# Optimization experiments

Hardware: AMD Instinct MI355X
Metric: run time of the kernel (lower is better)

Reference implementation:

```python
import jax, jax.numpy as jnp
import numpy as np

K = 3            # kernel size
PAD = 1          # padding for kernel_size=3
EPS = 1e-5       # BatchNorm eps
B, C, H, W = 8, 64, 256, 256


def deform_conv2d(x, offset, weight):
    """torchvision-style deform_conv2d, stride=1, pad=1, 1 offset group, no bias.
    x: [B, Cin, H, W]; offset: [B, 2*K*K, H, W] interleaved (dy, dx) per tap;
    weight: [Cout, Cin, K, K]."""
    b, cin, h, w = x.shape
    k2 = K * K
    off = offset.reshape(b, k2, 2, h, w)
    dy, dx = off[:, :, 0], off[:, :, 1]                 # [B,K2,H,W]
    kh = jnp.repeat(jnp.arange(K), K).astype(x.dtype)   # tap row, torch order k=kh*K+kw
    kw = jnp.tile(jnp.arange(K), K).astype(x.dtype)     # tap col
    # sampling positions: out pixel (i,j), tap k -> (i - PAD + kh + dy, j - PAD + kw + dx)
    py = dy + (jnp.arange(h, dtype=x.dtype) - PAD)[None, None, :, None] + kh[None, :, None, None]
    px = dx + (jnp.arange(w, dtype=x.dtype) - PAD)[None, None, None, :] + kw[None, :, None, None]

    y0 = jnp.floor(py); x0 = jnp.floor(px)
    wy = py - y0; wx = px - x0                          # bilinear fractions
    iy0 = y0.astype(jnp.int32); ix0 = x0.astype(jnp.int32)
    iy1 = iy0 + 1; ix1 = ix0 + 1

    xf = x.reshape(b, cin, h * w)

    def gather(iy, ix):
        valid = ((iy >= 0) & (iy < h) & (ix >= 0) & (ix < w)).astype(x.dtype)
        idx = jnp.clip(iy, 0, h - 1) * w + jnp.clip(ix, 0, w - 1)   # [B,K2,H,W]
        v = jax.vmap(lambda xi, ii: xi[:, ii])(xf, idx.reshape(b, -1))  # [B,Cin,K2*H*W]
        return v.reshape(b, cin, k2, h, w) * valid[:, None]

    sampled = ((1 - wy) * (1 - wx))[:, None] * gather(iy0, ix0) \
            + ((1 - wy) * wx)[:, None]       * gather(iy0, ix1) \
            + (wy * (1 - wx))[:, None]       * gather(iy1, ix0) \
            + (wy * wx)[:, None]             * gather(iy1, ix1)   # [B,Cin,K2,H,W]

    wk = weight.reshape(weight.shape[0], cin, k2)
    return jnp.einsum('bckhw,ock->bohw', sampled, wk)


def setup_inputs() -> dict:
    key = jax.random.key(0)
    k1, k2, k3 = jax.random.split(key, 3)
    x = jax.random.normal(k1, (B, C, H, W), dtype=jnp.float32)
    offset = jax.random.normal(k2, (B, 2 * K * K, H, W), dtype=jnp.float32)
    weight = jax.random.normal(k3, (1, 2, K, K), dtype=jnp.float32) * 0.1  # Conv2d(2,1,3)
    gamma = jnp.ones((1,), dtype=jnp.float32)
    beta = jnp.zeros((1,), dtype=jnp.float32)
    return {"x": x, "offset": offset, "weight": weight, "gamma": gamma, "beta": beta}


def reference(x, offset, weight, gamma, beta):
    avg_out = jnp.mean(x, axis=1, keepdims=True)
    max_out = jnp.max(x, axis=1, keepdims=True)
    feat = jnp.concatenate([avg_out, max_out], axis=1)      # [B,2,H,W]
    out = deform_conv2d(feat, offset, weight)               # [B,1,H,W]
    # BatchNorm2d (training-mode batch statistics)
    mu = jnp.mean(out, axis=(0, 2, 3), keepdims=True)
    var = jnp.var(out, axis=(0, 2, 3), keepdims=True)
    out = gamma.reshape(1, -1, 1, 1) * (out - mu) * jax.lax.rsqrt(var + EPS) + beta.reshape(1, -1, 1, 1)
    return x * jax.nn.sigmoid(out)
```

## Files before the change

### kernel.cpp

```cpp
#include <hip/hip_runtime.h>
#include <math.h>

#define BB 8
#define CC 64
#define HH 256
#define WW 256
#define HWp (HH * WW)
#define BHW (BB * HWp)
#define NK 9

typedef float f32x4 __attribute__((ext_vector_type(4)));

__global__ __launch_bounds__(256) void reduce_c_kernel(
    const float* __restrict__ x, float* __restrict__ feat, float* __restrict__ accum) {
    int t = blockIdx.x * 256 + threadIdx.x;
    if (blockIdx.x == 0 && threadIdx.x < 2) accum[threadIdx.x] = 0.f;
    int b = t / (HWp / 4);
    int p = t - b * (HWp / 4);
    const f32x4* xp = reinterpret_cast<const f32x4*>(x) + (size_t)b * CC * (HWp / 4) + p;
    f32x4 s = {0.f, 0.f, 0.f, 0.f};
    f32x4 m = {-INFINITY, -INFINITY, -INFINITY, -INFINITY};
#pragma unroll 16
    for (int c = 0; c < CC; ++c) {
        f32x4 v = xp[(size_t)c * (HWp / 4)];
        s += v;
        m.x = fmaxf(m.x, v.x); m.y = fmaxf(m.y, v.y);
        m.z = fmaxf(m.z, v.z); m.w = fmaxf(m.w, v.w);
    }
    const float inv = 1.0f / CC;
    f32x4 o0 = {s.x * inv, m.x, s.y * inv, m.y};
    f32x4 o1 = {s.z * inv, m.z, s.w * inv, m.w};
    f32x4* fp = reinterpret_cast<f32x4*>(feat) + 2 * (size_t)t;
    __builtin_nontemporal_store(o0, fp);
    __builtin_nontemporal_store(o1, fp + 1);
}

__device__ __forceinline__ float2 bisample(const float2* __restrict__ f, int iy, int ix) {
    bool v = ((unsigned)iy < (unsigned)HH) && ((unsigned)ix < (unsigned)WW);
    int cy = iy < 0 ? 0 : (iy > HH - 1 ? HH - 1 : iy);
    int cx = ix < 0 ? 0 : (ix > WW - 1 ? WW - 1 : ix);
    float2 r = f[cy * WW + cx];
    return v ? r : make_float2(0.f, 0.f);
}

__global__ __launch_bounds__(256) void dconv_kernel(
    const float* __restrict__ off, const float* __restrict__ wgt,
    const float* __restrict__ feat, float* __restrict__ outmap,
    float* __restrict__ accum) {
    int t = blockIdx.x * 256 + threadIdx.x;
    int b = t >> 16;
    int p = t & (HWp - 1);
    int h = p >> 8;
    int w = p & (WW - 1);

    const float* ob = off + (size_t)b * (2 * NK) * HWp + p;
    const float2* f = reinterpret_cast<const float2*>(feat) + (size_t)b * HWp;

    float wk[2 * NK];
#pragma unroll
    for (int i = 0; i < 2 * NK; ++i) wk[i] = wgt[i];

    float acc = 0.f;
#pragma unroll
    for (int k = 0; k < NK; ++k) {
        float dy = ob[(size_t)(2 * k) * HWp];
        float dx = ob[(size_t)(2 * k + 1) * HWp];
        float py = dy + (float)(h - 1 + k / 3);
        float px = dx + (float)(w - 1 + k % 3);
        float y0 = floorf(py), x0 = floorf(px);
        float wy = py - y0, wx = px - x0;
        int iy0 = (int)y0, ix0 = (int)x0;
        float w00 = (1.f - wy) * (1.f - wx);
        float w01 = (1.f - wy) * wx;
        float w10 = wy * (1.f - wx);
        float w11 = wy * wx;
        float2 c00 = bisample(f, iy0, ix0);
        float2 c01 = bisample(f, iy0, ix0 + 1);
        float2 c10 = bisample(f, iy0 + 1, ix0);
        float2 c11 = bisample(f, iy0 + 1, ix0 + 1);
        float s0 = w00 * c00.x + w01 * c01.x + w10 * c10.x + w11 * c11.x;
        float s1 = w00 * c00.y + w01 * c01.y + w10 * c10.y + w11 * c11.y;
        acc += wk[k] * s0 + wk[NK + k] * s1;
    }
    outmap[t] = acc;

    float s1r = acc, s2r = acc * acc;
#pragma unroll
    for (int o = 32; o > 0; o >>= 1) {
        s1r += __shfl_down(s1r, o, 64);
        s2r += __shfl_down(s2r, o, 64);
    }
    __shared__ float ls1[4], ls2[4];
    int lane = threadIdx.x & 63, wid = threadIdx.x >> 6;
    if (lane == 0) { ls1[wid] = s1r; ls2[wid] = s2r; }
    __syncthreads();
    if (threadIdx.x == 0) {
        float t1 = ls1[0] + ls1[1] + ls1[2] + ls1[3];
        float t2 = ls2[0] + ls2[1] + ls2[2] + ls2[3];
        atomicAdd(&accum[0], t1);
        atomicAdd(&accum[1], t2);
    }
}

__global__ __launch_bounds__(256) void sig_kernel(
    const float* __restrict__ outmap, const float* __restrict__ accum,
    const float* __restrict__ gamma, const float* __restrict__ beta,
    float* __restrict__ sigmap) {
    int t = blockIdx.x * 256 + threadIdx.x;
    float mu = accum[0] * (1.0f / BHW);
    float var = accum[1] * (1.0f / BHW) - mu * mu;
    float rs = rsqrtf(var + 1e-5f);
    float g = gamma[0], be = beta[0];
    f32x4 o = reinterpret_cast<const f32x4*>(outmap)[t];
    f32x4 r;
    r.x = 1.f / (1.f + expf(-(g * (o.x - mu) * rs + be)));
    r.y = 1.f / (1.f + expf(-(g * (o.y - mu) * rs + be)));
    r.z = 1.f / (1.f + expf(-(g * (o.z - mu) * rs + be)));
    r.w = 1.f / (1.f + expf(-(g * (o.w - mu) * rs + be)));
    reinterpret_cast<f32x4*>(sigmap)[t] = r;
}

__global__ __launch_bounds__(256) void final_kernel(
    const float* __restrict__ x, const float* __restrict__ sigmap,
    float* __restrict__ out) {
    size_t t = (size_t)blockIdx.x * 256 + threadIdx.x;
    const int per_b = CC * (HWp / 4);
    int b = (int)(t / per_b);
    int rem = (int)(t - (size_t)b * per_b);
    int p4 = rem & (HWp / 4 - 1);
    f32x4 xv = reinterpret_cast<const f32x4*>(x)[t];
    f32x4 sv = reinterpret_cast<const f32x4*>(sigmap)[b * (HWp / 4) + p4];
    f32x4 r = xv * sv;
    __builtin_nontemporal_store(r, reinterpret_cast<f32x4*>(out) + t);
}

extern "C" void kernel_launch(void* const* d_in, const int* in_sizes, int n_in,
                              void* d_out, int out_size, void* d_ws, size_t ws_size,
                              hipStream_t stream) {
    const float* x      = (const float*)d_in[0];
    const float* offset = (const float*)d_in[1];
    const float* weight = (const float*)d_in[2];
    const float* gamma  = (const float*)d_in[3];
    const float* beta   = (const float*)d_in[4];
    float* out = (float*)d_out;

    float* ws     = (float*)d_ws;
    float* feat   = ws;
    float* outmap = ws + 2 * BHW;
    float* accum  = ws + 3 * BHW;
    float* sigmap = feat;

    reduce_c_kernel<<<(BHW / 4) / 256, 256, 0, stream>>>(x, feat, accum);
    dconv_kernel<<<BHW / 256, 256, 0, stream>>>(offset, weight, feat, outmap, accum);
    sig_kernel<<<(BHW / 4) / 256, 256, 0, stream>>>(outmap, accum, gamma, beta, sigmap);
    final_kernel<<<((size_t)BB * CC * HWp / 4) / 256, 256, 0, stream>>>(x, sigmap, out);
}
```

Baseline: 334.0 us.

## Fuse four stage kernels into one persistent cooperative kernel with grid syncs

Merges the channel reduction, deformable conv with BN statistics, sigmoid and final multiply kernels into one cooperative persistent kernel. The stages are separated by grid-wide syncs and each uses grid-stride loops. The aim is to remove launch gaps between kernels and cut the atomics to one per block. In exchange it pays for the grid.sync barriers and a fixed grid of at most 1024 blocks, which may underfill the memory pipeline on streaming phases. It also drops the nontemporal store for feat.

```diff
diff --git a/kernel.cpp b/kernel.cpp
--- a/kernel.cpp
+++ b/kernel.cpp
@@ -1,5 +1,8 @@
 #include <hip/hip_runtime.h>
+#include <hip/hip_cooperative_groups.h>
 #include <math.h>
+
+namespace cg = cooperative_groups;
 
 #define BB 8
 #define CC 64
@@ -11,30 +14,6 @@
 
 typedef float f32x4 __attribute__((ext_vector_type(4)));
 
-__global__ __launch_bounds__(256) void reduce_c_kernel(
-    const float* __restrict__ x, float* __restrict__ feat, float* __restrict__ accum) {
-    int t = blockIdx.x * 256 + threadIdx.x;
-    if (blockIdx.x == 0 && threadIdx.x < 2) accum[threadIdx.x] = 0.f;
-    int b = t / (HWp / 4);
-    int p = t - b * (HWp / 4);
-    const f32x4* xp = reinterpret_cast<const f32x4*>(x) + (size_t)b * CC * (HWp / 4) + p;
-    f32x4 s = {0.f, 0.f, 0.f, 0.f};
-    f32x4 m = {-INFINITY, -INFINITY, -INFINITY, -INFINITY};
-#pragma unroll 16
-    for (int c = 0; c < CC; ++c) {
-        f32x4 v = xp[(size_t)c * (HWp / 4)];
-        s += v;
-        m.x = fmaxf(m.x, v.x); m.y = fmaxf(m.y, v.y);
-        m.z = fmaxf(m.z, v.z); m.w = fmaxf(m.w, v.w);
-    }
-    const float inv = 1.0f / CC;
-    f32x4 o0 = {s.x * inv, m.x, s.y * inv, m.y};
-    f32x4 o1 = {s.z * inv, m.z, s.w * inv, m.w};
-    f32x4* fp = reinterpret_cast<f32x4*>(feat) + 2 * (size_t)t;
-    __builtin_nontemporal_store(o0, fp);
-    __builtin_nontemporal_store(o1, fp + 1);
-}
-
 __device__ __forceinline__ float2 bisample(const float2* __restrict__ f, int iy, int ix) {
     bool v = ((unsigned)iy < (unsigned)HH) && ((unsigned)ix < (unsigned)WW);
     int cy = iy < 0 ? 0 : (iy > HH - 1 ? HH - 1 : iy);
@@ -43,95 +22,124 @@
     return v ? r : make_float2(0.f, 0.f);
 }
 
-__global__ __launch_bounds__(256) void dconv_kernel(
-    const float* __restrict__ off, const float* __restrict__ wgt,
-    const float* __restrict__ feat, float* __restrict__ outmap,
-    float* __restrict__ accum) {
-    int t = blockIdx.x * 256 + threadIdx.x;
-    int b = t >> 16;
-    int p = t & (HWp - 1);
-    int h = p >> 8;
-    int w = p & (WW - 1);
+__global__ __launch_bounds__(256, 4) void fused_kernel(
+    const float* __restrict__ x, const float* __restrict__ off,
+    const float* __restrict__ wgt, const float* __restrict__ gamma,
+    const float* __restrict__ beta, float* __restrict__ feat,
+    float* __restrict__ outmap, float* __restrict__ accum,
+    float* __restrict__ out) {
+    cg::grid_group grid = cg::this_grid();
+    const int gsize = gridDim.x * 256;
+    const int tid = blockIdx.x * 256 + threadIdx.x;
 
-    const float* ob = off + (size_t)b * (2 * NK) * HWp + p;
-    const float2* f = reinterpret_cast<const float2*>(feat) + (size_t)b * HWp;
+    if (tid < 2) accum[tid] = 0.f;
 
-    float wk[2 * NK];
+    for (int t = tid; t < BHW / 4; t += gsize) {
+        int b = t >> 14;
+        int p = t & (HWp / 4 - 1);
+        const f32x4* xp = reinterpret_cast<const f32x4*>(x) + (size_t)b * CC * (HWp / 4) + p;
+        f32x4 s = {0.f, 0.f, 0.f, 0.f};
+        f32x4 m = {-INFINITY, -INFINITY, -INFINITY, -INFINITY};
+#pragma unroll 16
+        for (int c = 0; c < CC; ++c) {
+            f32x4 v = xp[(size_t)c * (HWp / 4)];
+            s += v;
+            m.x = fmaxf(m.x, v.x); m.y = fmaxf(m.y, v.y);
+            m.z = fmaxf(m.z, v.z); m.w = fmaxf(m.w, v.w);
+        }
+        const float inv = 1.0f / CC;
+        f32x4 o0 = {s.x * inv, m.x, s.y * inv, m.y};
+        f32x4 o1 = {s.z * inv, m.z, s.w * inv, m.w};
+        f32x4* fp = reinterpret_cast<f32x4*>(feat) + 2 * (size_t)t;
+        fp[0] = o0;
+        fp[1] = o1;
+    }
+    grid.sync();
+
+    {
+        float wk[2 * NK];
 #pragma unroll
-    for (int i = 0; i < 2 * NK; ++i) wk[i] = wgt[i];
+        for (int i = 0; i < 2 * NK; ++i) wk[i] = wgt[i];
+        float s1r = 0.f, s2r = 0.f;
+        for (int t = tid; t < BHW; t += gsize) {
+            int b = t >> 16;
+            int p = t & (HWp - 1);
+            int h = p >> 8;
+            int w = p & (WW - 1);
+            const float* ob = off + (size_t)b * (2 * NK) * HWp + p;
+            const float2* f = reinterpret_cast<const float2*>(feat) + (size_t)b * HWp;
+            float acc = 0.f;
+#pragma unroll
+            for (int k = 0; k < NK; ++k) {
+                float dy = ob[(size_t)(2 * k) * HWp];
+                float dx = ob[(size_t)(2 * k + 1) * HWp];
+                float py = dy + (float)(h - 1 + k / 3);
+                float px = dx + (float)(w - 1 + k % 3);
+                float y0 = floorf(py), x0 = floorf(px);
+                float wy = py - y0, wx = px - x0;
+                int iy0 = (int)y0, ix0 = (int)x0;
+                float w00 = (1.f - wy) * (1.f - wx);
+                float w01 = (1.f - wy) * wx;
+                float w10 = wy * (1.f - wx);
+                float w11 = wy * wx;
+                float2 c00 = bisample(f, iy0, ix0);
+                float2 c01 = bisample(f, iy0, ix0 + 1);
+                float2 c10 = bisample(f, iy0 + 1, ix0);
+                float2 c11 = bisample(f, iy0 + 1, ix0 + 1);
+                float s0 = w00 * c00.x + w01 * c01.x + w10 * c10.x + w11 * c11.x;
+                float s1 = w00 * c00.y + w01 * c01.y + w10 * c10.y + w11 * c11.y;
+                acc += wk[k] * s0 + wk[NK + k] * s1;
+            }
+            outmap[t] = acc;
+            s1r += acc;
+            s2r += acc * acc;
+        }
+#pragma unroll
+        for (int o = 32; o > 0; o >>= 1) {
+            s1r += __shfl_down(s1r, o, 64);
+            s2r += __shfl_down(s2r, o, 64);
+        }
+        __shared__ float ls1[4], ls2[4];
+        int lane = threadIdx.x & 63, wid = threadIdx.x >> 6;
+        if (lane == 0) { ls1[wid] = s1r; ls2[wid] = s2r; }
+        __syncthreads();
+        if (threadIdx.x == 0) {
+            atomicAdd(&accum[0], ls1[0] + ls1[1] + ls1[2] + ls1[3]);
+            atomicAdd(&accum[1], ls2[0] + ls2[1] + ls2[2] + ls2[3]);
+        }
+    }
+    grid.sync();
 
-    float acc = 0.f;
-#pragma unroll
-    for (int k = 0; k < NK; ++k) {
-        float dy = ob[(size_t)(2 * k) * HWp];
-        float dx = ob[(size_t)(2 * k + 1) * HWp];
-        float py = dy + (float)(h - 1 + k / 3);
-        float px = dx + (float)(w - 1 + k % 3);
-        float y0 = floorf(py), x0 = floorf(px);
-        float wy = py - y0, wx = px - x0;
-        int iy0 = (int)y0, ix0 = (int)x0;
-        float w00 = (1.f - wy) * (1.f - wx);
-        float w01 = (1.f - wy) * wx;
-        float w10 = wy * (1.f - wx);
-        float w11 = wy * wx;
-        float2 c00 = bisample(f, iy0, ix0);
-        float2 c01 = bisample(f, iy0, ix0 + 1);
-        float2 c10 = bisample(f, iy0 + 1, ix0);
-        float2 c11 = bisample(f, iy0 + 1, ix0 + 1);
-        float s0 = w00 * c00.x + w01 * c01.x + w10 * c10.x + w11 * c11.x;
-        float s1 = w00 * c00.y + w01 * c01.y + w10 * c10.y + w11 * c11.y;
-        acc += wk[k] * s0 + wk[NK + k] * s1;
+    {
+        float mu = accum[0] * (1.0f / BHW);
+        float var = accum[1] * (1.0f / BHW) - mu * mu;
+        float rs = rsqrtf(var + 1e-5f);
+        float g = gamma[0], be = beta[0];
+        for (int t = tid; t < BHW / 4; t += gsize) {
+            f32x4 o = reinterpret_cast<const f32x4*>(outmap)[t];
+            f32x4 r;
+            r.x = 1.f / (1.f + expf(-(g * (o.x - mu) * rs + be)));
+            r.y = 1.f / (1.f + expf(-(g * (o.y - mu) * rs + be)));
+            r.z = 1.f / (1.f + expf(-(g * (o.z - mu) * rs + be)));
+            r.w = 1.f / (1.f + expf(-(g * (o.w - mu) * rs + be)));
+            reinterpret_cast<f32x4*>(feat)[t] = r;
+        }
     }
-    outmap[t] = acc;
+    grid.sync();
 
-    float s1r = acc, s2r = acc * acc;
-#pragma unroll
-    for (int o = 32; o > 0; o >>= 1) {
-        s1r += __shfl_down(s1r, o, 64);
-        s2r += __shfl_down(s2r, o, 64);
+    {
+        const float* __restrict__ sigmap = feat;
+        const int total = BB * CC * (HWp / 4);
+        for (int t = tid; t < total; t += gsize) {
+            int b = t >> 20;
+            int rem = t & ((CC * (HWp / 4)) - 1);
+            int p4 = rem & (HWp / 4 - 1);
+            f32x4 xv = reinterpret_cast<const f32x4*>(x)[(size_t)t];
+            f32x4 sv = reinterpret_cast<const f32x4*>(sigmap)[b * (HWp / 4) + p4];
+            f32x4 r = xv * sv;
+            __builtin_nontemporal_store(r, reinterpret_cast<f32x4*>(out) + t);
+        }
     }
-    __shared__ float ls1[4], ls2[4];
-    int lane = threadIdx.x & 63, wid = threadIdx.x >> 6;
-    if (lane == 0) { ls1[wid] = s1r; ls2[wid] = s2r; }
-    __syncthreads();
-    if (threadIdx.x == 0) {
-        float t1 = ls1[0] + ls1[1] + ls1[2] + ls1[3];
-        float t2 = ls2[0] + ls2[1] + ls2[2] + ls2[3];
-        atomicAdd(&accum[0], t1);
-        atomicAdd(&accum[1], t2);
-    }
-}
-
-__global__ __launch_bounds__(256) void sig_kernel(
-    const float* __restrict__ outmap, const float* __restrict__ accum,
-    const float* __restrict__ gamma, const float* __restrict__ beta,
-    float* __restrict__ sigmap) {
-    int t = blockIdx.x * 256 + threadIdx.x;
-    float mu = accum[0] * (1.0f / BHW);
-    float var = accum[1] * (1.0f / BHW) - mu * mu;
-    float rs = rsqrtf(var + 1e-5f);
-    float g = gamma[0], be = beta[0];
-    f32x4 o = reinterpret_cast<const f32x4*>(outmap)[t];
-    f32x4 r;
-    r.x = 1.f / (1.f + expf(-(g * (o.x - mu) * rs + be)));
-    r.y = 1.f / (1.f + expf(-(g * (o.y - mu) * rs + be)));
-    r.z = 1.f / (1.f + expf(-(g * (o.z - mu) * rs + be)));
-    r.w = 1.f / (1.f + expf(-(g * (o.w - mu) * rs + be)));
-    reinterpret_cast<f32x4*>(sigmap)[t] = r;
-}
-
-__global__ __launch_bounds__(256) void final_kernel(
-    const float* __restrict__ x, const float* __restrict__ sigmap,
-    float* __restrict__ out) {
-    size_t t = (size_t)blockIdx.x * 256 + threadIdx.x;
-    const int per_b = CC * (HWp / 4);
-    int b = (int)(t / per_b);
-    int rem = (int)(t - (size_t)b * per_b);
-    int p4 = rem & (HWp / 4 - 1);
-    f32x4 xv = reinterpret_cast<const f32x4*>(x)[t];
-    f32x4 sv = reinterpret_cast<const f32x4*>(sigmap)[b * (HWp / 4) + p4];
-    f32x4 r = xv * sv;
-    __builtin_nontemporal_store(r, reinterpret_cast<f32x4*>(out) + t);
 }
 
 extern "C" void kernel_launch(void* const* d_in, const int* in_sizes, int n_in,
@@ -148,10 +156,16 @@
     float* feat   = ws;
     float* outmap = ws + 2 * BHW;
     float* accum  = ws + 3 * BHW;
-    float* sigmap = feat;
 
-    reduce_c_kernel<<<(BHW / 4) / 256, 256, 0, stream>>>(x, feat, accum);
-    dconv_kernel<<<BHW / 256, 256, 0, stream>>>(offset, weight, feat, outmap, accum);
-    sig_kernel<<<(BHW / 4) / 256, 256, 0, stream>>>(outmap, accum, gamma, beta, sigmap);
-    final_kernel<<<((size_t)BB * CC * HWp / 4) / 256, 256, 0, stream>>>(x, sigmap, out);
+    int occ = 0;
+    hipOccupancyMaxActiveBlocksPerMultiprocessor(&occ, fused_kernel, 256, 0);
+    if (occ < 1) occ = 1;
+    int nblk = occ * 256;
+    if (nblk > 1024) nblk = 1024;
+
+    void* args[] = {(void*)&x, (void*)&offset, (void*)&weight, (void*)&gamma,
+                    (void*)&beta, (void*)&feat, (void*)&outmap, (void*)&accum,
+                    (void*)&out};
+    hipLaunchCooperativeKernel((const void*)fused_kernel, dim3(nblk), dim3(256),
+                               args, 0, stream);
 }
```

Measured after the change: 485.7 us. 1.45x slower.
